# Kernel optimization log

Hardware: AMD Instinct MI355X
Metric: run time of the kernel (lower is better)

Reference implementation:

```python
import jax, jax.numpy as jnp
import numpy as np
from jax import lax

EPS_BN = 1e-5
SMOOTH = 1e-5


def conv3x3(x, w):
    # x: [N,C,H,W], w: [O,I,3,3], stride 1, padding 1 (SAME)
    return lax.conv_general_dilated(
        x, w, window_strides=(1, 1), padding='SAME',
        dimension_numbers=('NCHW', 'OIHW', 'NCHW'))


def batchnorm(x, gamma, beta):
    # training-mode BatchNorm2d: batch statistics over (N,H,W), biased var
    mean = jnp.mean(x, axis=(0, 2, 3), keepdims=True)
    var = jnp.mean(jnp.square(x - mean), axis=(0, 2, 3), keepdims=True)
    g = gamma.reshape(1, -1, 1, 1)
    b = beta.reshape(1, -1, 1, 1)
    return (x - mean) * lax.rsqrt(var + EPS_BN) * g + b


def tanimoto(a, b, axes):
    tpl = jnp.sum(a * b, axis=axes, keepdims=True)
    sq = jnp.sum(a * a + b * b, axis=axes, keepdims=True)
    return (tpl + SMOOTH) / (sq - tpl + SMOOTH)


def tanimoto_compl(a, b, axes):
    return 0.5 * (tanimoto(a, b, axes) + tanimoto(1.0 - a, 1.0 - b, axes))


def setup_inputs() -> dict:
    key = jax.random.key(0)
    ks = jax.random.split(key, 5)
    N, Cin, Cout, H, W = 8, 64, 64, 256, 256
    x = jax.random.normal(ks[0], (N, Cin, H, W), dtype=jnp.float32)
    fan = Cin * 9
    wq = jax.random.normal(ks[1], (Cout, Cin, 3, 3), dtype=jnp.float32) / np.sqrt(fan)
    wk = jax.random.normal(ks[2], (Cout, Cin, 3, 3), dtype=jnp.float32) / np.sqrt(fan)
    wv = jax.random.normal(ks[3], (Cout, Cin, 3, 3), dtype=jnp.float32) / np.sqrt(fan)
    ones = jnp.ones((Cout,), dtype=jnp.float32)
    zeros = jnp.zeros((Cout,), dtype=jnp.float32)
    return {
        'x': x,
        'wq': wq, 'gq': ones, 'bq': zeros,
        'wk': wk, 'gk': ones, 'bk': zeros,
        'wv': wv, 'gv': ones, 'bv': zeros,
        'g_norm': ones, 'b_norm': zeros,
    }


def reference(x, wq, gq, bq, wk, gk, bk, wv, gv, bv, g_norm, b_norm):
    q = jax.nn.sigmoid(batchnorm(conv3x3(x, wq), gq, bq))
    k = jax.nn.sigmoid(batchnorm(conv3x3(x, wk), gk, bk))
    v = jax.nn.sigmoid(batchnorm(conv3x3(x, wv), gv, bv))
    attn_spatial = tanimoto_compl(q, k, axes=(1,))      # [N,1,H,W]
    attn_channel = tanimoto_compl(q, k, axes=(2, 3))    # [N,C,1,1]
    attention = 0.5 * (attn_spatial * v + attn_channel * v)
    return batchnorm(attention, g_norm, b_norm)
```

## Files before the change

kernel.cpp:

```cpp
#include <hip/hip_runtime.h>

typedef unsigned short u16;
typedef __attribute__((ext_vector_type(8))) short short8;
typedef __attribute__((ext_vector_type(4))) float f32x4;
typedef __attribute__((ext_vector_type(16))) float f32x16;

#define OFF_SUMS 0ul
#define OFF_WT   26624ul
#define OFF_ASP  247808ul
#define OFF_CONV 2344960ul
#define S_SUM   0
#define S_SSQ   768
#define M_A1    1920
#define M_A23   2432
#define M_A45   2944
#define M_V1    3456
#define M_V2    3968
#define M_AV    4480
#define M_AV2   4992
#define M_A2V2  5504
#define S_NFLOAT 6656

__device__ __forceinline__ float bf2f(u16 v) {
  union { unsigned u; float f; } x; x.u = ((unsigned)v) << 16; return x.f;
}
__device__ __forceinline__ u16 f2bf(float f) {
  union { float f; unsigned u; } x; x.f = f;
  unsigned r = x.u + 0x7fffu + ((x.u >> 16) & 1u);
  return (u16)(r >> 16);
}
__device__ __forceinline__ float frcp(float x) { return __builtin_amdgcn_rcpf(x); }
__device__ __forceinline__ float sigmoidf_(float x) { return frcp(1.f + __expf(-x)); }

template <int CTRL, int RMASK>
__device__ __forceinline__ float dpp_add(float x) {
  int m = __builtin_amdgcn_update_dpp(0, __builtin_bit_cast(int, x), CTRL, RMASK, 0xf, true);
  return x + __builtin_bit_cast(float, m);
}
__device__ __forceinline__ float wsum64(float x) {
  x = dpp_add<0x111, 0xf>(x);
  x = dpp_add<0x112, 0xf>(x);
  x = dpp_add<0x114, 0xf>(x);
  x = dpp_add<0x118, 0xf>(x);
  x = dpp_add<0x142, 0xa>(x);
  x = dpp_add<0x143, 0xc>(x);
  return __builtin_bit_cast(float, __builtin_amdgcn_readlane(__builtin_bit_cast(int, x), 63));
}

__global__ void tr_k(const float* __restrict__ x, u16* __restrict__ xt,
                     const float* __restrict__ wq, const float* __restrict__ wk,
                     const float* __restrict__ wv, u16* __restrict__ wt,
                     float* __restrict__ S) {
  const int bid = blockIdx.x;
  const int tid = threadIdx.x;
  if (bid == 4536) {
    for (int i = tid; i < S_NFLOAT; i += 256) S[i] = 0.f;
    return;
  }
  if (bid >= 4104) {
    int i = (bid - 4104) * 256 + tid;
    if (i >= 110592) return;
    int j = i & 7, l = (i >> 3) & 63, kc = (i >> 9) & 3;
    int t2 = i >> 11;
    int ocg = t2 % 6, dydx = t2 / 6;
    int oc = ocg * 32 + (l & 31);
    int ch = kc * 16 + (l >> 5) * 8 + j;
    int cs = oc >> 6, ol = oc & 63;
    const float* src = cs == 0 ? wq : (cs == 1 ? wk : wv);
    wt[i] = f2bf(src[(ol * 64 + ch) * 9 + dydx]);
    return;
  }
  if (bid >= 4096) {
    const int n = bid - 4096;
    const uint4 z = make_uint4(0u, 0u, 0u, 0u);
    for (int t = tid; t < 8224; t += 256) {
      int cell = t >> 3, g = t & 7;
      int row, col;
      if (cell < 258) { row = 0; col = cell; }
      else if (cell < 516) { row = 257; col = cell - 258; }
      else if (cell < 772) { row = cell - 516 + 1; col = 0; }
      else { row = cell - 772 + 1; col = 257; }
      *(uint4*)(xt + ((long)(n * 258 + row) * 258 + col) * 64 + (g << 3)) = z;
    }
    return;
  }
  __shared__ u16 t[64][130];
  const int wtile = bid & 1, h = (bid >> 1) & 255, n = bid >> 9;
  const int w0 = wtile << 7;
#pragma unroll
  for (int it = 0; it < 8; ++it) {
    int i = it * 256 + tid;
    int c = i >> 5, w4 = (i & 31) << 2;
    const f32x4 v = *(const f32x4*)(&x[(((long)((n << 6) + c)) << 16) + (h << 8) + w0 + w4]);
    unsigned p0 = (unsigned)f2bf(v[0]) | ((unsigned)f2bf(v[1]) << 16);
    unsigned p1 = (unsigned)f2bf(v[2]) | ((unsigned)f2bf(v[3]) << 16);
    *(unsigned*)(&t[c][w4]) = p0;
    *(unsigned*)(&t[c][w4 + 2]) = p1;
  }
  __syncthreads();
#pragma unroll
  for (int it = 0; it < 4; ++it) {
    int i = it * 256 + tid;
    int g = i & 7, w = i >> 3;
    int c8 = g << 3;
    unsigned short u[8];
#pragma unroll
    for (int j = 0; j < 8; ++j) u[j] = t[c8 + j][w];
    uint4 val;
    val.x = (unsigned)u[0] | ((unsigned)u[1] << 16);
    val.y = (unsigned)u[2] | ((unsigned)u[3] << 16);
    val.z = (unsigned)u[4] | ((unsigned)u[5] << 16);
    val.w = (unsigned)u[6] | ((unsigned)u[7] << 16);
    const int pw = w0 + w + 1;
    const int gs = g ^ (pw & 7);
    *(uint4*)(xt + ((long)(n * 258 + h + 1) * 258 + pw) * 64 + (gs << 3)) = val;
  }
}

__global__ __launch_bounds__(256, 2) void conv_k(const u16* __restrict__ xt,
                                                 const u16* __restrict__ wt,
                                                 u16* __restrict__ conv,
                                                 float* __restrict__ S) {
  __shared__ u16 lx[3 * 8704];
  const int bid = blockIdx.x;
  const int wtile = bid & 1, h = (bid >> 1) & 255, n = bid >> 9;
  const int w0 = wtile << 7;
  const int tid = threadIdx.x;
  const int lane = tid & 63, wave = tid >> 6;
  const int l31 = lane & 31, half = lane >> 5;
  const int wm = wave & 1, wn = wave >> 1;
  {
    const long rowbase = ((long)(n * 258 + h) * 258 + w0) * 64;
    for (int c = wave; c < 51; c += 4) {
      const int s = (c >= 34) ? 2 : (c >= 17 ? 1 : 0);
      const int lc = c - s * 17;
      const int loff = s * 8704 + lc * 512 + lane * 8;
      const long goff = rowbase + (long)s * 16512 + lc * 512 + lane * 8;
      __builtin_amdgcn_global_load_lds(
          (const __attribute__((address_space(1))) unsigned int*)(xt + goff),
          (__attribute__((address_space(3))) unsigned int*)(&lx[loff]), 16, 0, 0);
    }
  }
  short8 bfr0[3][4];
#pragma unroll
  for (int nt = 0; nt < 3; ++nt)
#pragma unroll
    for (int kc = 0; kc < 4; ++kc)
      bfr0[nt][kc] = *(const short8*)(wt + ((wn * 3 + nt) * 4 + kc) * 512 + lane * 8);
  __syncthreads();
  f32x16 acc[3][2];
#pragma unroll
  for (int a = 0; a < 3; ++a)
#pragma unroll
    for (int b = 0; b < 2; ++b)
#pragma unroll
      for (int e = 0; e < 16; ++e) acc[a][b][e] = 0.f;

#pragma unroll
  for (int dy = 0; dy < 3; ++dy) {
#pragma unroll
    for (int dx = 0; dx < 3; ++dx) {
      const u16* wp = wt + (dy * 3 + dx) * 12288;
      short8 bfr[3][4];
#pragma unroll
      for (int nt = 0; nt < 3; ++nt)
#pragma unroll
        for (int kc = 0; kc < 4; ++kc)
          bfr[nt][kc] = (dy == 0 && dx == 0) ? bfr0[nt][kc]
                        : *(const short8*)(wp + ((wn * 3 + nt) * 4 + kc) * 512 + lane * 8);
#pragma unroll
      for (int kc = 0; kc < 4; ++kc) {
        short8 afr[2];
#pragma unroll
        for (int mt = 0; mt < 2; ++mt) {
          const int px = wm * 64 + mt * 32 + l31 + dx;
          const int chb = kc * 16 + half * 8;
          int idx = ((px << 6) + chb) ^ ((px & 7) << 3);
          afr[mt] = *(const short8*)(&lx[dy * 8704 + idx]);
        }
#pragma unroll
        for (int mt = 0; mt < 2; ++mt)
#pragma unroll
          for (int nt = 0; nt < 3; ++nt)
            acc[nt][mt] = __builtin_amdgcn_mfma_f32_32x32x16_bf16(afr[mt], bfr[nt][kc], acc[nt][mt], 0, 0, 0);
      }
    }
  }
  const long pix0 = (long)bid * 128 + wm * 64;
#pragma unroll
  for (int nt = 0; nt < 3; ++nt) {
    const int oc = wn * 96 + nt * 32 + l31;
#pragma unroll
    for (int mt = 0; mt < 2; ++mt) {
      const long pxb = pix0 + mt * 32 + half * 4;
#pragma unroll
      for (int rq = 0; rq < 4; ++rq)
#pragma unroll
        for (int rr = 0; rr < 4; ++rr) {
          const long px = pxb + rr + 8 * rq;
          conv[px * 192 + oc] = f2bf(acc[nt][mt][rq * 4 + rr]);
        }
    }
  }
  const int sh = (bid & 3) * 192;
#pragma unroll
  for (int nt = 0; nt < 3; ++nt) {
    float s = 0.f, ss = 0.f;
#pragma unroll
    for (int mt = 0; mt < 2; ++mt)
#pragma unroll
      for (int r = 0; r < 16; ++r) {
        float x = acc[nt][mt][r];
        s += x; ss += x * x;
      }
    s += __shfl_xor(s, 32); ss += __shfl_xor(ss, 32);
    if (lane < 32) {
      const int oc = wn * 96 + nt * 32 + lane;
      atomicAdd(&S[S_SUM + sh + oc], s);
      atomicAdd(&S[S_SSQ + sh + oc], ss);
    }
  }
}

__global__ void k3_k(const u16* __restrict__ conv, float* __restrict__ S, float* __restrict__ asp,
                     const float* __restrict__ gq, const float* __restrict__ bq,
                     const float* __restrict__ gk, const float* __restrict__ bk,
                     const float* __restrict__ gv, const float* __restrict__ bv) {
  __shared__ float red[4][8][64];
  __shared__ float scb[192], bib[192];
  const int tid = threadIdx.x, lane = tid & 63, wave = tid >> 6;
  const int bid = blockIdx.x;
  const int n = bid >> 9;
  const long p0 = (long)bid * 128 + wave * 32;
  if (tid < 192) {
    int cv = tid >> 6, c = tid & 63;
    float g = cv == 0 ? gq[c] : (cv == 1 ? gk[c] : gv[c]);
    float b = cv == 0 ? bq[c] : (cv == 1 ? bk[c] : bv[c]);
    float sm = 0.f, sq2 = 0.f;
#pragma unroll
    for (int sh = 0; sh < 4; ++sh) { sm += S[S_SUM + sh * 192 + tid]; sq2 += S[S_SSQ + sh * 192 + tid]; }
    const float inv = 1.f / 524288.f;
    float mean = sm * inv;
    float var = sq2 * inv - mean * mean;
    float rstd = rsqrtf(var + 1e-5f);
    float sc = g * rstd;
    scb[tid] = sc;
    bib[tid] = b - mean * sc;
  }
  __syncthreads();
  const float sq = scb[lane], bq_ = bib[lane];
  const float sk = scb[64 + lane], bk_ = bib[64 + lane];
  const float sv = scb[128 + lane], bv_ = bib[128 + lane];
  float A1 = 0.f, A23 = 0.f, A45 = 0.f, V1 = 0.f, V2 = 0.f, AV = 0.f, AV2 = 0.f, A2V2 = 0.f;
  float myasp = 0.f;
#pragma unroll 4
  for (int i = 0; i < 32; ++i) {
    const u16* row = conv + (p0 + i) * 192;
    float q = sigmoidf_(bf2f(row[lane]) * sq + bq_);
    float k = sigmoidf_(bf2f(row[64 + lane]) * sk + bk_);
    float v = sigmoidf_(bf2f(row[128 + lane]) * sv + bv_);
    float p1 = q * k, p23 = q * q + k * k, p45 = q + k;
    A1 += p1; A23 += p23; A45 += p45;
    float s1 = wsum64(p1);
    float s23 = wsum64(p23);
    float s45 = wsum64(p45);
    const float sm = 1e-5f;
    float t1 = (s1 + sm) * frcp(s23 - s1 + sm);
    float t2 = (64.f - s45 + s1 + sm) * frcp(64.f - s45 + s23 - s1 + sm);
    float a = 0.5f * (t1 + t2);
    if (i == (lane & 31)) myasp = a;
    float av = a * v;
    V1 += v; V2 += v * v; AV += av; AV2 += av * v; A2V2 += av * av;
  }
  if (lane < 32) asp[p0 + lane] = myasp;
  red[wave][0][lane] = A1;  red[wave][1][lane] = A23; red[wave][2][lane] = A45;
  red[wave][3][lane] = V1;  red[wave][4][lane] = V2;  red[wave][5][lane] = AV;
  red[wave][6][lane] = AV2; red[wave][7][lane] = A2V2;
  __syncthreads();
  if (tid < 64) {
    const int mb[8] = {M_A1, M_A23, M_A45, M_V1, M_V2, M_AV, M_AV2, M_A2V2};
#pragma unroll
    for (int m = 0; m < 8; ++m) {
      float t = red[0][m][tid] + red[1][m][tid] + red[2][m][tid] + red[3][m][tid];
      atomicAdd(&S[mb[m] + n * 64 + tid], t);
    }
  }
}

__global__ void k6_k(const u16* __restrict__ conv, const float* __restrict__ S,
                     const float* __restrict__ asp, float* __restrict__ out,
                     const float* __restrict__ gv, const float* __restrict__ bv,
                     const float* __restrict__ gn, const float* __restrict__ bn_) {
  __shared__ float t[128][65];
  __shared__ float svv[64], bvv[64], achb[64], sAv[64], bAv[64];
  const int tid = threadIdx.x, lane = tid & 63, wave = tid >> 6;
  const int n = blockIdx.x >> 9;
  const int hw0 = (blockIdx.x & 511) << 7;
  const long P0 = (long)blockIdx.x * 128;
  if (tid < 64) {
    const float inv = 1.f / 524288.f;
    float sm = 0.f, sq2 = 0.f;
#pragma unroll
    for (int sh = 0; sh < 4; ++sh) {
      sm += S[S_SUM + sh * 192 + 128 + tid];
      sq2 += S[S_SSQ + sh * 192 + 128 + tid];
    }
    float mean = sm * inv;
    float var = sq2 * inv - mean * mean;
    float rstd = rsqrtf(var + 1e-5f);
    float sv = gv[tid] * rstd;
    svv[tid] = sv;
    bvv[tid] = bv[tid] - mean * sv;
    const float smc = 1e-5f, cnt = 65536.f;
    float s1 = 0.f, s2 = 0.f, myach = 0.f;
#pragma unroll
    for (int nn = 0; nn < 8; ++nn) {
      int idx = nn * 64 + tid;
      float A1 = S[M_A1 + idx], A23 = S[M_A23 + idx], A45 = S[M_A45 + idx];
      float t1 = (A1 + smc) / (A23 - A1 + smc);
      float t2 = (cnt - A45 + A1 + smc) / (cnt - A45 + A23 - A1 + smc);
      float ach = 0.5f * (t1 + t2);
      if (nn == n) myach = ach;
      s1 += 0.5f * (S[M_AV + idx] + ach * S[M_V1 + idx]);
      s2 += 0.25f * (S[M_A2V2 + idx] + 2.f * ach * S[M_AV2 + idx] + ach * ach * S[M_V2 + idx]);
    }
    float mean2 = s1 * inv;
    float var2 = s2 * inv - mean2 * mean2;
    float rstd2 = rsqrtf(var2 + 1e-5f);
    float sA = gn[tid] * rstd2;
    sAv[tid] = sA;
    bAv[tid] = bn_[tid] - mean2 * sA;
    achb[tid] = myach;
  }
  __syncthreads();
  const float sv = svv[lane], bvx = bvv[lane];
  const float av = achb[lane];
  const float sA = sAv[lane], bA = bAv[lane];
  for (int i = wave; i < 128; i += 4) {
    const long p = P0 + i;
    float v = sigmoidf_(bf2f(conv[p * 192 + 128 + lane]) * sv + bvx);
    float att = 0.5f * (asp[p] + av) * v;
    t[i][lane] = att * sA + bA;
  }
  __syncthreads();
  const int c0 = tid >> 3, sub = tid & 7;
#pragma unroll
  for (int cl = 0; cl < 2; ++cl) {
    const int c = c0 + 32 * cl;
    const long plane = ((long)((n << 6) + c)) << 16;
#pragma unroll
    for (int i = 0; i < 4; ++i) {
      const int pst = (i * 8 + sub) << 2;
      f32x4 vbuf;
#pragma unroll
      for (int j = 0; j < 4; ++j) vbuf[j] = t[pst + j][c];
      *(f32x4*)(&out[plane + hw0 + pst]) = vbuf;
    }
  }
}

extern "C" void kernel_launch(void* const* d_in, const int* in_sizes, int n_in,
                              void* d_out, int out_size, void* d_ws, size_t ws_size,
                              hipStream_t stream) {
  (void)in_sizes; (void)n_in; (void)out_size; (void)ws_size;
  const float* x  = (const float*)d_in[0];
  const float* wq = (const float*)d_in[1];
  const float* gq = (const float*)d_in[2];
  const float* bq = (const float*)d_in[3];
  const float* wk = (const float*)d_in[4];
  const float* gk = (const float*)d_in[5];
  const float* bk = (const float*)d_in[6];
  const float* wv = (const float*)d_in[7];
  const float* gv = (const float*)d_in[8];
  const float* bv = (const float*)d_in[9];
  const float* gn = (const float*)d_in[10];
  const float* bn_ = (const float*)d_in[11];
  char* ws = (char*)d_ws;
  float* S   = (float*)(ws + OFF_SUMS);
  u16* wt    = (u16*)(ws + OFF_WT);
  float* asp = (float*)(ws + OFF_ASP);
  u16* conv  = (u16*)(ws + OFF_CONV);
  float* out = (float*)d_out;
  u16* xt  = (u16*)d_out;

  tr_k<<<4537, 256, 0, stream>>>(x, xt, wq, wk, wv, wt, S);
  conv_k<<<4096, 256, 0, stream>>>(xt, wt, conv, S);
  k3_k<<<4096, 256, 0, stream>>>(conv, S, asp, gq, bq, gk, bk, gv, bv);
  k6_k<<<4096, 256, 0, stream>>>(conv, S, asp, out, gv, bv, gn, bn_);
}
```

Baseline: 537.1 us.

## Vectorize k3/k6 conv reads with 8-channel per-lane layout and segmented DPP sums

Reworks the statistics kernel and the final output kernel so each lane handles 8 consecutive channels of one pixel, loading them with 16-byte vector loads instead of scalar 2-byte loads. The per-pixel channel reduction becomes an in-lane sum plus a 3-step DPP reduction over 8 lanes, replacing three full 64-lane DPP+readlane reductions per pixel. Partial channel accumulators are reduced through a larger shared-memory buffer, and the k6 transpose tile gets padding of 68 so it can take vector stores. The cost is more registers (8-wide accumulator arrays) and possible LDS bank conflicts in the new layouts.

```diff
diff --git a/kernel.cpp b/kernel.cpp
--- a/kernel.cpp
+++ b/kernel.cpp
@@ -37,14 +37,11 @@
   int m = __builtin_amdgcn_update_dpp(0, __builtin_bit_cast(int, x), CTRL, RMASK, 0xf, true);
   return x + __builtin_bit_cast(float, m);
 }
-__device__ __forceinline__ float wsum64(float x) {
-  x = dpp_add<0x111, 0xf>(x);
-  x = dpp_add<0x112, 0xf>(x);
-  x = dpp_add<0x114, 0xf>(x);
-  x = dpp_add<0x118, 0xf>(x);
-  x = dpp_add<0x142, 0xa>(x);
-  x = dpp_add<0x143, 0xc>(x);
-  return __builtin_bit_cast(float, __builtin_amdgcn_readlane(__builtin_bit_cast(int, x), 63));
+__device__ __forceinline__ float seg8sum(float x) {
+  x = dpp_add<0xB1, 0xf>(x);
+  x = dpp_add<0x4E, 0xf>(x);
+  x = dpp_add<0x141, 0xf>(x);
+  return x;
 }
 
 __global__ void tr_k(const float* __restrict__ x, u16* __restrict__ xt,
@@ -226,15 +223,16 @@
                      const float* __restrict__ gq, const float* __restrict__ bq,
                      const float* __restrict__ gk, const float* __restrict__ bk,
                      const float* __restrict__ gv, const float* __restrict__ bv) {
-  __shared__ float red[4][8][64];
   __shared__ float scb[192], bib[192];
+  __shared__ float mred[4][4][8][8][8];
   const int tid = threadIdx.x, lane = tid & 63, wave = tid >> 6;
   const int bid = blockIdx.x;
   const int n = bid >> 9;
+  const int g = lane >> 3, cs = lane & 7;
   const long p0 = (long)bid * 128 + wave * 32;
   if (tid < 192) {
     int cv = tid >> 6, c = tid & 63;
-    float g = cv == 0 ? gq[c] : (cv == 1 ? gk[c] : gv[c]);
+    float gg = cv == 0 ? gq[c] : (cv == 1 ? gk[c] : gv[c]);
     float b = cv == 0 ? bq[c] : (cv == 1 ? bk[c] : bv[c]);
     float sm = 0.f, sq2 = 0.f;
 #pragma unroll
@@ -243,45 +241,82 @@
     float mean = sm * inv;
     float var = sq2 * inv - mean * mean;
     float rstd = rsqrtf(var + 1e-5f);
-    float sc = g * rstd;
+    float sc = gg * rstd;
     scb[tid] = sc;
     bib[tid] = b - mean * sc;
   }
   __syncthreads();
-  const float sq = scb[lane], bq_ = bib[lane];
-  const float sk = scb[64 + lane], bk_ = bib[64 + lane];
-  const float sv = scb[128 + lane], bv_ = bib[128 + lane];
-  float A1 = 0.f, A23 = 0.f, A45 = 0.f, V1 = 0.f, V2 = 0.f, AV = 0.f, AV2 = 0.f, A2V2 = 0.f;
-  float myasp = 0.f;
-#pragma unroll 4
-  for (int i = 0; i < 32; ++i) {
-    const u16* row = conv + (p0 + i) * 192;
-    float q = sigmoidf_(bf2f(row[lane]) * sq + bq_);
-    float k = sigmoidf_(bf2f(row[64 + lane]) * sk + bk_);
-    float v = sigmoidf_(bf2f(row[128 + lane]) * sv + bv_);
-    float p1 = q * k, p23 = q * q + k * k, p45 = q + k;
-    A1 += p1; A23 += p23; A45 += p45;
-    float s1 = wsum64(p1);
-    float s23 = wsum64(p23);
-    float s45 = wsum64(p45);
+  float sq[8], bq2[8], sk[8], bk2[8], sv[8], bv2[8];
+#pragma unroll
+  for (int j = 0; j < 8; ++j) {
+    sq[j] = scb[cs * 8 + j];        bq2[j] = bib[cs * 8 + j];
+    sk[j] = scb[64 + cs * 8 + j];   bk2[j] = bib[64 + cs * 8 + j];
+    sv[j] = scb[128 + cs * 8 + j];  bv2[j] = bib[128 + cs * 8 + j];
+  }
+  float A1[8], A23[8], A45[8], V1[8], V2[8], AV[8], AV2[8], A2V2[8];
+#pragma unroll
+  for (int j = 0; j < 8; ++j) {
+    A1[j] = A23[j] = A45[j] = V1[j] = V2[j] = AV[j] = AV2[j] = A2V2[j] = 0.f;
+  }
+#pragma unroll
+  for (int i = 0; i < 4; ++i) {
+    const long p = p0 + i * 8 + g;
+    const u16* row = conv + p * 192;
+    short8 qv = *(const short8*)(row + cs * 8);
+    short8 kv = *(const short8*)(row + 64 + cs * 8);
+    short8 vv = *(const short8*)(row + 128 + cs * 8);
+    float s1l = 0.f, s23l = 0.f, s45l = 0.f;
+    float vf[8];
+#pragma unroll
+    for (int j = 0; j < 8; ++j) {
+      float qf = sigmoidf_(bf2f((u16)qv[j]) * sq[j] + bq2[j]);
+      float kf = sigmoidf_(bf2f((u16)kv[j]) * sk[j] + bk2[j]);
+      vf[j] = sigmoidf_(bf2f((u16)vv[j]) * sv[j] + bv2[j]);
+      float p1 = qf * kf, p23 = qf * qf + kf * kf, p45 = qf + kf;
+      A1[j] += p1; A23[j] += p23; A45[j] += p45;
+      s1l += p1; s23l += p23; s45l += p45;
+    }
+    float s1 = seg8sum(s1l);
+    float s23 = seg8sum(s23l);
+    float s45 = seg8sum(s45l);
     const float sm = 1e-5f;
     float t1 = (s1 + sm) * frcp(s23 - s1 + sm);
     float t2 = (64.f - s45 + s1 + sm) * frcp(64.f - s45 + s23 - s1 + sm);
     float a = 0.5f * (t1 + t2);
-    if (i == (lane & 31)) myasp = a;
-    float av = a * v;
-    V1 += v; V2 += v * v; AV += av; AV2 += av * v; A2V2 += av * av;
-  }
-  if (lane < 32) asp[p0 + lane] = myasp;
-  red[wave][0][lane] = A1;  red[wave][1][lane] = A23; red[wave][2][lane] = A45;
-  red[wave][3][lane] = V1;  red[wave][4][lane] = V2;  red[wave][5][lane] = AV;
-  red[wave][6][lane] = AV2; red[wave][7][lane] = A2V2;
+    if (cs == 0) asp[p] = a;
+#pragma unroll
+    for (int j = 0; j < 8; ++j) {
+      float v = vf[j], av = a * v;
+      V1[j] += v; V2[j] += v * v; AV[j] += av; AV2[j] += av * v; A2V2[j] += av * av;
+    }
+  }
+#pragma unroll
+  for (int j = 0; j < 8; ++j) {
+    A1[j] = dpp_add<0x128, 0xf>(A1[j]);   A23[j] = dpp_add<0x128, 0xf>(A23[j]);
+    A45[j] = dpp_add<0x128, 0xf>(A45[j]); V1[j] = dpp_add<0x128, 0xf>(V1[j]);
+    V2[j] = dpp_add<0x128, 0xf>(V2[j]);   AV[j] = dpp_add<0x128, 0xf>(AV[j]);
+    AV2[j] = dpp_add<0x128, 0xf>(AV2[j]); A2V2[j] = dpp_add<0x128, 0xf>(A2V2[j]);
+  }
+  if ((g & 1) == 0) {
+    float* dst = &mred[wave][g >> 1][cs][0][0];
+#pragma unroll
+    for (int j = 0; j < 8; ++j) {
+      dst[0 * 8 + j] = A1[j];  dst[1 * 8 + j] = A23[j]; dst[2 * 8 + j] = A45[j];
+      dst[3 * 8 + j] = V1[j];  dst[4 * 8 + j] = V2[j];  dst[5 * 8 + j] = AV[j];
+      dst[6 * 8 + j] = AV2[j]; dst[7 * 8 + j] = A2V2[j];
+    }
+  }
   __syncthreads();
   if (tid < 64) {
     const int mb[8] = {M_A1, M_A23, M_A45, M_V1, M_V2, M_AV, M_AV2, M_A2V2};
+    const int csf = tid >> 3, jf = tid & 7;
 #pragma unroll
     for (int m = 0; m < 8; ++m) {
-      float t = red[0][m][tid] + red[1][m][tid] + red[2][m][tid] + red[3][m][tid];
+      float t = 0.f;
+#pragma unroll
+      for (int w = 0; w < 4; ++w)
+#pragma unroll
+        for (int gh = 0; gh < 4; ++gh) t += mred[w][gh][csf][m][jf];
       atomicAdd(&S[mb[m] + n * 64 + tid], t);
     }
   }
@@ -291,7 +326,7 @@
                      const float* __restrict__ asp, float* __restrict__ out,
                      const float* __restrict__ gv, const float* __restrict__ bv,
                      const float* __restrict__ gn, const float* __restrict__ bn_) {
-  __shared__ float t[128][65];
+  __shared__ float t[128][68];
   __shared__ float svv[64], bvv[64], achb[64], sAv[64], bAv[64];
   const int tid = threadIdx.x, lane = tid & 63, wave = tid >> 6;
   const int n = blockIdx.x >> 9;
@@ -333,14 +368,29 @@
     achb[tid] = myach;
   }
   __syncthreads();
-  const float sv = svv[lane], bvx = bvv[lane];
-  const float av = achb[lane];
-  const float sA = sAv[lane], bA = bAv[lane];
-  for (int i = wave; i < 128; i += 4) {
-    const long p = P0 + i;
-    float v = sigmoidf_(bf2f(conv[p * 192 + 128 + lane]) * sv + bvx);
-    float att = 0.5f * (asp[p] + av) * v;
-    t[i][lane] = att * sA + bA;
+  const int g = lane >> 3, cs = lane & 7;
+  float sv8[8], bv8[8], av8[8], sA8[8], bA8[8];
+#pragma unroll
+  for (int j = 0; j < 8; ++j) {
+    int c = cs * 8 + j;
+    sv8[j] = svv[c]; bv8[j] = bvv[c]; av8[j] = achb[c]; sA8[j] = sAv[c]; bA8[j] = bAv[c];
+  }
+#pragma unroll
+  for (int i = 0; i < 4; ++i) {
+    const int px = i * 32 + wave * 8 + g;
+    const long p = P0 + px;
+    short8 vv = *(const short8*)(conv + p * 192 + 128 + cs * 8);
+    float aspv = asp[p];
+    f32x4 lo, hi;
+#pragma unroll
+    for (int j = 0; j < 8; ++j) {
+      float v = sigmoidf_(bf2f((u16)vv[j]) * sv8[j] + bv8[j]);
+      float att = 0.5f * (aspv + av8[j]) * v;
+      float o = att * sA8[j] + bA8[j];
+      if (j < 4) lo[j] = o; else hi[j - 4] = o;
+    }
+    *(f32x4*)(&t[px][cs * 8]) = lo;
+    *(f32x4*)(&t[px][cs * 8 + 4]) = hi;
   }
   __syncthreads();
   const int c0 = tid >> 3, sub = tid & 7;
```

Result: slower. 572.6 us (+6.6%).

## Remap k3 stats kernel so each lane handles four channels of four pixels

Applied to the files above, without the earlier changes.

The channel-statistics kernel now gives each 16-lane group a different pixel, with each lane covering four contiguous channels through vector bf16 loads. The full-wave DPP reduction plus readlane is replaced by a four-step 16-lane segmented reduction, cutting cross-lane work and the serial loop trip count from 32 to 8. Per-channel accumulators become four-wide arrays, and the block reduction goes through a larger shared buffer summed over 16 groups. Launch bounds are added. The cost is more registers and a longer final shared-memory reduction.

```diff
diff --git a/kernel.cpp b/kernel.cpp
--- a/kernel.cpp
+++ b/kernel.cpp
@@ -1,6 +1,7 @@
 #include <hip/hip_runtime.h>
 
 typedef unsigned short u16;
+typedef __attribute__((ext_vector_type(4))) short short4v;
 typedef __attribute__((ext_vector_type(8))) short short8;
 typedef __attribute__((ext_vector_type(4))) float f32x4;
 typedef __attribute__((ext_vector_type(16))) float f32x16;
@@ -37,14 +38,12 @@
   int m = __builtin_amdgcn_update_dpp(0, __builtin_bit_cast(int, x), CTRL, RMASK, 0xf, true);
   return x + __builtin_bit_cast(float, m);
 }
-__device__ __forceinline__ float wsum64(float x) {
-  x = dpp_add<0x111, 0xf>(x);
-  x = dpp_add<0x112, 0xf>(x);
-  x = dpp_add<0x114, 0xf>(x);
-  x = dpp_add<0x118, 0xf>(x);
-  x = dpp_add<0x142, 0xa>(x);
-  x = dpp_add<0x143, 0xc>(x);
-  return __builtin_bit_cast(float, __builtin_amdgcn_readlane(__builtin_bit_cast(int, x), 63));
+__device__ __forceinline__ float seg16sum(float x) {
+  x = dpp_add<0xB1, 0xf>(x);
+  x = dpp_add<0x4E, 0xf>(x);
+  x = dpp_add<0x141, 0xf>(x);
+  x = dpp_add<0x140, 0xf>(x);
+  return x;
 }
 
 __global__ void tr_k(const float* __restrict__ x, u16* __restrict__ xt,
@@ -222,19 +221,21 @@
   }
 }
 
-__global__ void k3_k(const u16* __restrict__ conv, float* __restrict__ S, float* __restrict__ asp,
+__global__ __launch_bounds__(256, 4) void k3_k(const u16* __restrict__ conv, float* __restrict__ S,
+                     float* __restrict__ asp,
                      const float* __restrict__ gq, const float* __restrict__ bq,
                      const float* __restrict__ gk, const float* __restrict__ bk,
                      const float* __restrict__ gv, const float* __restrict__ bv) {
-  __shared__ float red[4][8][64];
   __shared__ float scb[192], bib[192];
+  __shared__ float mred[16][16][36];
   const int tid = threadIdx.x, lane = tid & 63, wave = tid >> 6;
   const int bid = blockIdx.x;
   const int n = bid >> 9;
+  const int g = lane >> 4, cs = lane & 15;
   const long p0 = (long)bid * 128 + wave * 32;
   if (tid < 192) {
     int cv = tid >> 6, c = tid & 63;
-    float g = cv == 0 ? gq[c] : (cv == 1 ? gk[c] : gv[c]);
+    float gg = cv == 0 ? gq[c] : (cv == 1 ? gk[c] : gv[c]);
     float b = cv == 0 ? bq[c] : (cv == 1 ? bk[c] : bv[c]);
     float sm = 0.f, sq2 = 0.f;
 #pragma unroll
@@ -243,45 +244,75 @@
     float mean = sm * inv;
     float var = sq2 * inv - mean * mean;
     float rstd = rsqrtf(var + 1e-5f);
-    float sc = g * rstd;
+    float sc = gg * rstd;
     scb[tid] = sc;
     bib[tid] = b - mean * sc;
   }
   __syncthreads();
-  const float sq = scb[lane], bq_ = bib[lane];
-  const float sk = scb[64 + lane], bk_ = bib[64 + lane];
-  const float sv = scb[128 + lane], bv_ = bib[128 + lane];
-  float A1 = 0.f, A23 = 0.f, A45 = 0.f, V1 = 0.f, V2 = 0.f, AV = 0.f, AV2 = 0.f, A2V2 = 0.f;
-  float myasp = 0.f;
-#pragma unroll 4
-  for (int i = 0; i < 32; ++i) {
-    const u16* row = conv + (p0 + i) * 192;
-    float q = sigmoidf_(bf2f(row[lane]) * sq + bq_);
-    float k = sigmoidf_(bf2f(row[64 + lane]) * sk + bk_);
-    float v = sigmoidf_(bf2f(row[128 + lane]) * sv + bv_);
-    float p1 = q * k, p23 = q * q + k * k, p45 = q + k;
-    A1 += p1; A23 += p23; A45 += p45;
-    float s1 = wsum64(p1);
-    float s23 = wsum64(p23);
-    float s45 = wsum64(p45);
+  float sq[4], bq2[4], sk[4], bk2[4], sv[4], bv2[4];
+#pragma unroll
+  for (int j = 0; j < 4; ++j) {
+    sq[j] = scb[cs * 4 + j];        bq2[j] = bib[cs * 4 + j];
+    sk[j] = scb[64 + cs * 4 + j];   bk2[j] = bib[64 + cs * 4 + j];
+    sv[j] = scb[128 + cs * 4 + j];  bv2[j] = bib[128 + cs * 4 + j];
+  }
+  float A1[4], A23[4], A45[4], V1[4], V2[4], AV[4], AV2[4], A2V2[4];
+#pragma unroll
+  for (int j = 0; j < 4; ++j) {
+    A1[j] = A23[j] = A45[j] = V1[j] = V2[j] = AV[j] = AV2[j] = A2V2[j] = 0.f;
+  }
+#pragma unroll
+  for (int i = 0; i < 8; ++i) {
+    const long p = p0 + i * 4 + g;
+    const u16* row = conv + p * 192;
+    short4v qv = *(const short4v*)(row + cs * 4);
+    short4v kv = *(const short4v*)(row + 64 + cs * 4);
+    short4v vv = *(const short4v*)(row + 128 + cs * 4);
+    float s1l = 0.f, s23l = 0.f, s45l = 0.f;
+    float vf[4];
+#pragma unroll
+    for (int j = 0; j < 4; ++j) {
+      float qf = sigmoidf_(bf2f((u16)qv[j]) * sq[j] + bq2[j]);
+      float kf = sigmoidf_(bf2f((u16)kv[j]) * sk[j] + bk2[j]);
+      vf[j] = sigmoidf_(bf2f((u16)vv[j]) * sv[j] + bv2[j]);
+      float p1 = qf * kf, p23 = qf * qf + kf * kf, p45 = qf + kf;
+      A1[j] += p1; A23[j] += p23; A45[j] += p45;
+      s1l += p1; s23l += p23; s45l += p45;
+    }
+    float s1 = seg16sum(s1l);
+    float s23 = seg16sum(s23l);
+    float s45 = seg16sum(s45l);
     const float sm = 1e-5f;
     float t1 = (s1 + sm) * frcp(s23 - s1 + sm);
     float t2 = (64.f - s45 + s1 + sm) * frcp(64.f - s45 + s23 - s1 + sm);
     float a = 0.5f * (t1 + t2);
-    if (i == (lane & 31)) myasp = a;
-    float av = a * v;
-    V1 += v; V2 += v * v; AV += av; AV2 += av * v; A2V2 += av * av;
-  }
-  if (lane < 32) asp[p0 + lane] = myasp;
-  red[wave][0][lane] = A1;  red[wave][1][lane] = A23; red[wave][2][lane] = A45;
-  red[wave][3][lane] = V1;  red[wave][4][lane] = V2;  red[wave][5][lane] = AV;
-  red[wave][6][lane] = AV2; red[wave][7][lane] = A2V2;
+    if (cs == 0) asp[p] = a;
+#pragma unroll
+    for (int j = 0; j < 4; ++j) {
+      float v = vf[j], av = a * v;
+      V1[j] += v; V2[j] += v * v; AV[j] += av; AV2[j] += av * v; A2V2[j] += av * av;
+    }
+  }
+  {
+    float* dst = &mred[wave * 4 + g][cs][0];
+    *(f32x4*)(dst + 0)  = (f32x4){A1[0], A1[1], A1[2], A1[3]};
+    *(f32x4*)(dst + 4)  = (f32x4){A23[0], A23[1], A23[2], A23[3]};
+    *(f32x4*)(dst + 8)  = (f32x4){A45[0], A45[1], A45[2], A45[3]};
+    *(f32x4*)(dst + 12) = (f32x4){V1[0], V1[1], V1[2], V1[3]};
+    *(f32x4*)(dst + 16) = (f32x4){V2[0], V2[1], V2[2], V2[3]};
+    *(f32x4*)(dst + 20) = (f32x4){AV[0], AV[1], AV[2], AV[3]};
+    *(f32x4*)(dst + 24) = (f32x4){AV2[0], AV2[1], AV2[2], AV2[3]};
+    *(f32x4*)(dst + 28) = (f32x4){A2V2[0], A2V2[1], A2V2[2], A2V2[3]};
+  }
   __syncthreads();
   if (tid < 64) {
     const int mb[8] = {M_A1, M_A23, M_A45, M_V1, M_V2, M_AV, M_AV2, M_A2V2};
+    const int csf = tid >> 2, jf = tid & 3;
 #pragma unroll
     for (int m = 0; m < 8; ++m) {
-      float t = red[0][m][tid] + red[1][m][tid] + red[2][m][tid] + red[3][m][tid];
+      float t = 0.f;
+#pragma unroll
+      for (int wg = 0; wg < 16; ++wg) t += mred[wg][csf][m * 4 + jf];
       atomicAdd(&S[mb[m] + n * 64 + tid], t);
     }
   }
```

Result: slower. 568.8 us (+5.9%).
